# Performance work log

Measured on AMD Instinct MI355X. Metric: run time of the kernel, lower is better.

## Reference

```python
import jax, jax.numpy as jnp
import numpy as np

B, N_SIDE, S = 64, 40, 512
N = N_SIDE * N_SIDE          # 1600 grid points (fl_feature_dims [1,40,40])
EMB = 10                     # embedding_dim
GDIM = 8                     # lie('homography').dim
WIDTH = 128
C1 = 20                      # first-layer output channels


def _embed(x, emb_dim):
    # sinusoidal embedding of each scalar coordinate: [..., D] -> [..., D*emb_dim]
    freqs = 2.0 ** jnp.arange(emb_dim // 2, dtype=x.dtype)
    ang = x[..., None] * freqs                       # [..., D, emb/2]
    e = jnp.concatenate([jnp.sin(ang), jnp.cos(ang)], axis=-1)  # [..., D, emb]
    return e.reshape(x.shape[:-1] + (x.shape[-1] * emb_dim,))


def _glorot(key, shape):
    fan_in = shape[0]
    return jax.random.normal(key, shape, dtype=jnp.float32) / np.sqrt(fan_in)


def setup_inputs() -> dict:
    key = jax.random.key(0)
    ks = jax.random.split(key, 16)
    inp = {
        'data':   jax.random.normal(ks[0], (B, N, 1), dtype=jnp.float32),
        'v0':     jax.random.normal(ks[1], (S, GDIM), dtype=jnp.float32),
        'v_last': jax.random.normal(ks[2], (S, GDIM), dtype=jnp.float32),
        # FirstLayer filter MLP: 2*EMB -> 20 -> 20 -> 1*C1
        'fl_w1': _glorot(ks[3], (2 * EMB, 20)), 'fl_b1': jnp.zeros((20,), jnp.float32),
        'fl_w2': _glorot(ks[4], (20, 20)),      'fl_b2': jnp.zeros((20,), jnp.float32),
        'fl_w3': _glorot(ks[5], (20, C1)),      'fl_b3': jnp.zeros((C1,), jnp.float32),
        # Hidden FilterMLP: EMB*GDIM=80 -> WIDTH -> C1*WIDTH
        's_w1': _glorot(ks[6], (EMB * GDIM, WIDTH)), 's_b1': jnp.zeros((WIDTH,), jnp.float32),
        's_w2': _glorot(ks[7], (WIDTH, C1 * WIDTH)), 's_b2': jnp.zeros((C1 * WIDTH,), jnp.float32),
        'fc1_w': _glorot(ks[8], (WIDTH, WIDTH)), 'fc1_b': jnp.zeros((WIDTH,), jnp.float32),
        'fc2_w': _glorot(ks[9], (WIDTH, WIDTH)), 'fc2_b': jnp.zeros((WIDTH,), jnp.float32),
        'pool_w': _glorot(ks[10], (WIDTH, 10)),  'pool_b': jnp.zeros((10,), jnp.float32),
    }
    return inp


def reference(data, v0, v_last, fl_w1, fl_b1, fl_w2, fl_b2, fl_w3, fl_b3,
              s_w1, s_b1, s_w2, s_b2, fc1_w, fc1_b, fc2_w, fc2_b, pool_w, pool_b):
    silu = jax.nn.silu
    # pixel grid in [-1,1]^2, homogeneous coords [N,3]
    lin = jnp.linspace(-1.0, 1.0, N_SIDE, dtype=data.dtype)
    xx, yy = jnp.meshgrid(lin, lin, indexing='ij')
    coords = jnp.stack([xx.ravel(), yy.ravel()], axis=-1)           # [N,2]
    xh = jnp.concatenate([coords, jnp.ones((N, 1), data.dtype)], -1)  # [N,3]
    # homography matrices: identity + small perturbation from 8 group params
    pert = jnp.concatenate([0.1 * v_last, jnp.zeros((S, 1), data.dtype)], -1).reshape(S, 3, 3)
    H = jnp.eye(3, dtype=data.dtype) + pert                          # [S,3,3]
    y = jnp.einsum('sij,nj->sni', H, xh)                             # [S,N,3]
    t = y[..., :2] / y[..., 2:3]                                     # projective action [S,N,2]
    # continuous-kernel first layer: filters generated by MLP on embedded coords
    e1 = _embed(t, EMB)                                              # [S,N,20]
    h = silu(e1 @ fl_w1 + fl_b1)
    h = silu(h @ fl_w2 + fl_b2)
    filt1 = h @ fl_w3 + fl_b3                                        # [S,N,C1]
    z = jnp.einsum('bn,sno->bso', data[:, :, 0], filt1) / N          # [B,S,C1]
    z = silu(z)
    # hidden FilterMLP on group samples v0 -> per-sample filters [S,C1,WIDTH]
    v0e = _embed(v0, EMB)                                            # [S,80]
    h2 = silu(v0e @ s_w1 + s_b1)                                     # [S,WIDTH]
    filt2 = (h2 @ s_w2 + s_b2).reshape(S, C1, WIDTH)
    # (1/S) * sum over group-sample and channel axes of broadcast product
    z = jnp.einsum('bsc,scw->bw', z, filt2) / S                      # [B,WIDTH]
    z = silu(z @ fc1_w + fc1_b) + z
    z = silu(z @ fc2_w + fc2_b) + z
    return z @ pool_w + pool_b                                       # [B,10]
```

## Files before the change

### kernel.cpp

```cpp
#include <hip/hip_runtime.h>

#define N_PTS 1600
#define NSIDE 40
#define SNUM  512
#define BNUM  64
#define C1D   20
#define WID   128

typedef _Float16 h8  __attribute__((ext_vector_type(8)));
typedef _Float16 h4  __attribute__((ext_vector_type(4)));
typedef __fp16   h2v __attribute__((ext_vector_type(2)));
typedef float    f4  __attribute__((ext_vector_type(4)));

__device__ __forceinline__ float silu_f(float x){
    return x * __builtin_amdgcn_rcpf(1.f + __expf(-x));
}
__device__ __forceinline__ void fma4(float4& a, float s, const float4 w){
    a.x += s*w.x; a.y += s*w.y; a.z += s*w.z; a.w += s*w.w;
}

__global__ __launch_bounds__(256) void ka_prep(
    const float* __restrict__ data, const float* __restrict__ v0,
    const float* __restrict__ s_w1, const float* __restrict__ s_b1,
    const float* __restrict__ s_w2, const float* __restrict__ s_b2,
    const float* __restrict__ w1, const float* __restrict__ b1,
    const float* __restrict__ w2, const float* __restrict__ b2,
    const float* __restrict__ w3, const float* __restrict__ b3,
    _Float16* __restrict__ dataA, float* __restrict__ f2g,
    _Float16* __restrict__ wPackA, float* __restrict__ bPackA,
    float* __restrict__ out2g)
{
    const int t  = threadIdx.x;
    const int bx = blockIdx.x;
    if (bx == 690) {
        const float* wsrc[3] = { w1, w2, w3 };
        const float* bsrc[3] = { b1, b2, b3 };
        for (int v = t; v < 3072; v += 256) {
            const int l = v >> 10, rem = v & 1023;
            const int cout = rem >> 5, cin = rem & 31;
            float x = 0.f;
            if (cout < 20 && cin < 20) x = wsrc[l][cin * 20 + cout];
            wPackA[v] = (_Float16)x;
        }
        if (t < 96) {
            const int l = t >> 5, cout = t & 31;
            bPackA[t] = (cout < 20) ? bsrc[l][cout] : 0.f;
        }
        for (int v = t; v < 8192; v += 256) out2g[v] = 0.f;
        return;
    }
    if (bx >= 640) {
        const int o  = (bx - 640) * 256 + t;
        const int L  = o & 63, cm = o >> 6;
        const int mt = cm & 3, ch = cm >> 2;
        const int b  = mt * 16 + (L & 15);
        const int nb = ch * 32 + (L >> 4) * 8;
        const float* src = data + b * N_PTS + nb;
        h8 v;
        #pragma unroll
        for (int j = 0; j < 8; j++) v[j] = (_Float16)src[j];
        *(h8*)(dataA + (size_t)o * 8) = v;
        return;
    }
    const int st  = bx / 10, ct = bx - st * 10;
    const int s0  = st * 8;
    const int col = ct * 256 + t;
    __shared__ __align__(16) float h2t[128][12];
    __shared__ __align__(16) float svt[8][8][10];

    if (t < 64) {
        const int ss = t >> 3, d = t & 7;
        const float val = v0[(s0 + ss) * 8 + d];
        float sv, cv;
        __sincosf(val, &sv, &cv);
        #pragma unroll
        for (int k = 0; k < 5; k++) {
            svt[ss][d][k]     = sv;
            svt[ss][d][5 + k] = cv;
            const float ns = 2.f * sv * cv;
            const float nc = 1.f - 2.f * sv * sv;
            sv = ns; cv = nc;
        }
    }
    __syncthreads();

    {
        const int j  = t & 127;
        const int sh = t >> 7;
        float hacc[4];
        const float bias1 = s_b1[j];
        #pragma unroll
        for (int u = 0; u < 4; u++) hacc[u] = bias1;
        for (int d = 0; d < 8; d++) {
            #pragma unroll
            for (int kk = 0; kk < 10; kk++) {
                const float wv = s_w1[(d * 10 + kk) * WID + j];
                #pragma unroll
                for (int u = 0; u < 4; u++)
                    hacc[u] += svt[sh * 4 + u][d][kk] * wv;
            }
        }
        #pragma unroll
        for (int u = 0; u < 4; u++) h2t[j][sh * 4 + u] = silu_f(hacc[u]);
    }
    __syncthreads();

    float4 acc[2];
    acc[0] = make_float4(0.f, 0.f, 0.f, 0.f);
    acc[1] = make_float4(0.f, 0.f, 0.f, 0.f);
    #pragma unroll 4
    for (int i = 0; i < 128; i++) {
        const float wv = s_w2[i * 2560 + col];
        const float4* hh = (const float4*)&h2t[i][0];
        fma4(acc[0], wv, hh[0]);
        fma4(acc[1], wv, hh[1]);
    }
    const float bias = s_b2[col];
    const float* af = (const float*)acc;
    #pragma unroll
    for (int ss = 0; ss < 8; ss++)
        f2g[(s0 + ss) * 2560 + col] = af[ss] + bias;
}

__device__ __forceinline__ void embed_coord(
    int n, float hA, float hB, float hC, float h6, float h7, float h8c,
    h2v e5[5])
{
    const int i = n / NSIDE;
    const int j = n - i * NSIDE;
    const float x = -1.f + (float)i * (2.f/39.f);
    const float y = -1.f + (float)j * (2.f/39.f);
    const float yc = hA*x + hB*y + hC;
    const float y2 = h6*x + h7*y + h8c;
    const float tc = yc * __builtin_amdgcn_rcpf(y2);
    float e[10];
    float sv, cv;
    __sincosf(tc, &sv, &cv);
    #pragma unroll
    for (int k = 0; k < 5; k++) {
        e[k] = sv; e[5+k] = cv;
        const float ns = 2.f*sv*cv, nc = 1.f - 2.f*sv*sv; sv = ns; cv = nc;
    }
    #pragma unroll
    for (int k = 0; k < 5; k++)
        e5[k] = __builtin_amdgcn_cvt_pkrtz(e[2*k], e[2*k+1]);
}

#define ASTRIDE 40

__global__ __launch_bounds__(512, 8) void kf_filt(
    const float* __restrict__ v_last,
    const _Float16* __restrict__ wPackA, const float* __restrict__ bPackA,
    _Float16* __restrict__ filtG)
{
    const int s    = blockIdx.x & 511;
    const int half = blockIdx.x >> 9;
    const int nb0  = half * 800;
    const int t    = threadIdx.x;
    const int lane = t & 63;
    const int w    = t >> 6;
    const int q    = lane >> 4;
    const int l15  = lane & 15;
    const int ep   = lane >> 1;
    const int ec   = lane & 1;
    const int erow = w*16 + ep + ((ep >> 4) * 112);

    __shared__ __align__(16) _Float16 act[256 * ASTRIDE];
    __shared__ __align__(16) _Float16 wlds[3072];
    __shared__ __align__(16) float    blds[96];

    for (int v = t; v < 1536; v += 512)
        ((unsigned int*)wlds)[v] = ((const unsigned int*)wPackA)[v];
    if (t < 96) blds[t] = bPackA[t];

    float Hm[9];
    #pragma unroll
    for (int k = 0; k < 9; k++) Hm[k] = (k == 0 || k == 4 || k == 8) ? 1.f : 0.f;
    #pragma unroll
    for (int k = 0; k < 8; k++) Hm[k] += 0.1f * v_last[s*8 + k];
    const float hA = ec ? Hm[3] : Hm[0];
    const float hB = ec ? Hm[4] : Hm[1];
    const float hC = ec ? Hm[5] : Hm[2];

    if (ec == 0) {
        unsigned long long* pz = (unsigned long long*)(act + erow*ASTRIDE + 20);
        pz[0] = 0ull; pz[1] = 0ull; pz[2] = 0ull;
    }

    __syncthreads();

    _Float16* fgs = filtG + (size_t)(half*512 + s) * 16000;

    for (int base = 0; base < 800; base += 256) {
        const int tn = min(256, 800 - base);

        if (erow < tn) {
            h2v e5[5];
            embed_coord(nb0 + base + erow, hA, hB, hC, Hm[6], Hm[7], Hm[8], e5);
            #pragma unroll
            for (int k = 0; k < 5; k++)
                *(h2v*)(act + erow*ASTRIDE + ec*10 + 2*k) = e5[k];
        }

        const int nmt = tn >> 4;
        #pragma unroll
        for (int l = 0; l < 3; l++) {
            const h8 wf0 = *(const h8*)(wlds + ((l*2+0)*16 + l15) * 32 + q*8);
            const h8 wf1 = *(const h8*)(wlds + ((l*2+1)*16 + l15) * 32 + q*8);
            const float b0 = blds[(l*2+0)*16 + l15];
            const float b1 = blds[(l*2+1)*16 + l15];
            const f4 zero4 = (f4)(0.f);
            for (int mt = w; mt < nmt; mt += 8) {
                const int r0 = mt * 16;
                const h8 af = *(const h8*)(act + (r0 + l15)*ASTRIDE + q*8);
                f4 D0 = __builtin_amdgcn_mfma_f32_16x16x32_f16(af, wf0, zero4, 0, 0, 0);
                f4 D1 = __builtin_amdgcn_mfma_f32_16x16x32_f16(af, wf1, zero4, 0, 0, 0);
                if (l < 2) {
                    #pragma unroll
                    for (int r = 0; r < 4; r++) {
                        const int p = r0 + q*4 + r;
                        act[p*ASTRIDE + l15] = (_Float16)silu_f(D0[r] + b0);
                        if (l15 < 4)
                            act[p*ASTRIDE + 16 + l15] = (_Float16)silu_f(D1[r] + b1);
                    }
                } else {
                    h4 p0, p1;
                    #pragma unroll
                    for (int r = 0; r < 4; r++) {
                        p0[r] = (_Float16)(D0[r] + b0);
                        p1[r] = (_Float16)(D1[r] + b1);
                    }
                    *(h4*)(fgs + l15*800 + base + r0 + q*4) = p0;
                    if (l15 < 4)
                        *(h4*)(fgs + (16 + l15)*800 + base + r0 + q*4) = p1;
                }
            }
        }
    }
}

__global__ __launch_bounds__(256, 6) void kz_gemm(
    const _Float16* __restrict__ dataA, const _Float16* __restrict__ filtG,
    float* __restrict__ zpart)
{
    const int s    = blockIdx.x & 511;
    const int half = blockIdx.x >> 9;
    const int t    = threadIdx.x;
    const int lane = t & 63;
    const int w    = t >> 6;
    const int q    = lane >> 4;
    const int l15  = lane & 15;

    __shared__ __align__(16) float red[4 * 64 * 21];

    const _Float16* fgs = filtG + (size_t)(half*512 + s) * 16000;
    const int r1row = (l15 < 4) ? (16 + l15) : 0;

    f4 zacc[4][2];
    #pragma unroll
    for (int mt = 0; mt < 4; mt++) { zacc[mt][0] = (f4)(0.f); zacc[mt][1] = (f4)(0.f); }

    for (int kc = w; kc < 25; kc += 4) {
        const h8 bf0 = *(const h8*)(fgs + l15  *800 + kc*32 + q*8);
        const h8 bf1 = *(const h8*)(fgs + r1row*800 + kc*32 + q*8);
        const int gchunk = half*25 + kc;
        #pragma unroll
        for (int mt = 0; mt < 4; mt++) {
            const h8 afz = *(const h8*)(dataA + ((size_t)(gchunk*4 + mt)*64 + lane)*8);
            zacc[mt][0] = __builtin_amdgcn_mfma_f32_16x16x32_f16(afz, bf0, zacc[mt][0], 0, 0, 0);
            zacc[mt][1] = __builtin_amdgcn_mfma_f32_16x16x32_f16(afz, bf1, zacc[mt][1], 0, 0, 0);
        }
    }

    #pragma unroll
    for (int mt = 0; mt < 4; mt++) {
        #pragma unroll
        for (int r = 0; r < 4; r++) {
            const int b = mt*16 + q*4 + r;
            red[(w*64 + b)*21 + l15] = zacc[mt][0][r];
            if (l15 < 4) red[(w*64 + b)*21 + 16 + l15] = zacc[mt][1][r];
        }
    }
    __syncthreads();
    for (int v = t; v < 1280; v += 256) {
        const int c = v >> 6, b = v & 63;
        const float sum = red[(      b)*21 + c] + red[( 64 + b)*21 + c]
                        + red[(128 + b)*21 + c] + red[(192 + b)*21 + c];
        zpart[(half*512 + s)*1280 + v] = sum;
    }
}

__global__ __launch_bounds__(256) void k2_contract(
    const float* __restrict__ zg, const float* __restrict__ f2g,
    float* __restrict__ out2g)
{
    const int blk = blockIdx.x;
    const int sg  = blk >> 1;
    const int wh  = blk & 1;
    const int s0  = sg * 4;
    const int w0  = wh * 64;
    const int t   = threadIdx.x;
    __shared__ __align__(16) float zl[4*1280];
    __shared__ __align__(16) float fl[4*20*64];
    #pragma unroll
    for (int sp = 0; sp < 4; sp++) {
        const int srow = (s0 + sp) * 1280;
        for (int r = t; r < 1280; r += 256) {
            const float a0 = zg[srow + r];
            const float a1 = zg[512*1280 + srow + r];
            zl[sp*1280 + r] = silu_f((a0 + a1) * (1.f / (float)N_PTS));
        }
        for (int u = t; u < 1280; u += 256) {
            const int c = u >> 6, ww = u & 63;
            fl[sp*1280 + u] = f2g[(s0 + sp)*2560 + c*128 + w0 + ww];
        }
    }
    __syncthreads();
    const int ww = t & 63, bh = t >> 6;
    float4 acc[4];
    #pragma unroll
    for (int qq = 0; qq < 4; qq++) acc[qq] = make_float4(0.f, 0.f, 0.f, 0.f);
    #pragma unroll 4
    for (int sc = 0; sc < 80; sc++) {
        const float f = fl[sc * 64 + ww];
        const float4* zz = (const float4*)&zl[sc * 64 + bh * 16];
        #pragma unroll
        for (int qq = 0; qq < 4; qq++) fma4(acc[qq], f, zz[qq]);
    }
    const float* af = (const float*)acc;
    #pragma unroll
    for (int idx = 0; idx < 16; idx++) {
        const int b = bh * 16 + idx;
        atomicAdd(&out2g[b * 128 + w0 + ww], af[idx]);
    }
}

__global__ __launch_bounds__(128) void k3_tail(
    const float* __restrict__ out2g,
    const float* __restrict__ fc1w, const float* __restrict__ fc1b,
    const float* __restrict__ fc2w, const float* __restrict__ fc2b,
    const float* __restrict__ pw,   const float* __restrict__ pb,
    float* __restrict__ out)
{
    const int b = blockIdx.x, t = threadIdx.x;
    __shared__ float zb[128], r1[128], r2[128];
    zb[t] = out2g[b * 128 + t] * (1.f / (float)SNUM);
    __syncthreads();
    float a = fc1b[t];
    #pragma unroll 8
    for (int i = 0; i < 128; i++) a += zb[i] * fc1w[i * 128 + t];
    r1[t] = silu_f(a) + zb[t];
    __syncthreads();
    a = fc2b[t];
    #pragma unroll 8
    for (int i = 0; i < 128; i++) a += r1[i] * fc2w[i * 128 + t];
    r2[t] = silu_f(a) + r1[t];
    __syncthreads();
    if (t < 10) {
        float o = pb[t];
        #pragma unroll 8
        for (int i = 0; i < 128; i++) o += r2[i] * pw[i * 10 + t];
        out[b * 10 + t] = o;
    }
}

extern "C" void kernel_launch(void* const* d_in, const int* in_sizes, int n_in,
                              void* d_out, int out_size, void* d_ws, size_t ws_size,
                              hipStream_t stream) {
    const float* data   = (const float*)d_in[0];
    const float* v0     = (const float*)d_in[1];
    const float* v_last = (const float*)d_in[2];
    const float* fl_w1  = (const float*)d_in[3];
    const float* fl_b1  = (const float*)d_in[4];
    const float* fl_w2  = (const float*)d_in[5];
    const float* fl_b2  = (const float*)d_in[6];
    const float* fl_w3  = (const float*)d_in[7];
    const float* fl_b3  = (const float*)d_in[8];
    const float* s_w1   = (const float*)d_in[9];
    const float* s_b1   = (const float*)d_in[10];
    const float* s_w2   = (const float*)d_in[11];
    const float* s_b2   = (const float*)d_in[12];
    const float* fc1_w  = (const float*)d_in[13];
    const float* fc1_b  = (const float*)d_in[14];
    const float* fc2_w  = (const float*)d_in[15];
    const float* fc2_b  = (const float*)d_in[16];
    const float* pool_w = (const float*)d_in[17];
    const float* pool_b = (const float*)d_in[18];
    float* out = (float*)d_out;

    float* ws        = (float*)d_ws;
    _Float16* dataA  = (_Float16*)ws;
    float* zpart  = ws    + 51200;
    float* f2g    = zpart + 1310720;
    float* out2g  = f2g   + 1310720;
    _Float16* wPackA = (_Float16*)(out2g + 8192);
    float* bPackA = out2g + 8192 + 1536;
    _Float16* filtG = (_Float16*)(bPackA + 96);

    ka_prep    <<<691, 256, 0, stream>>>(data, v0, s_w1, s_b1, s_w2, s_b2,
                                         fl_w1, fl_b1, fl_w2, fl_b2, fl_w3, fl_b3,
                                         dataA, f2g, wPackA, bPackA, out2g);
    kf_filt    <<<1024, 512, 0, stream>>>(v_last, wPackA, bPackA, filtG);
    kz_gemm    <<<1024, 256, 0, stream>>>(dataA, filtG, zpart);
    k2_contract<<<256, 256, 0, stream>>>(zpart, f2g, out2g);
    k3_tail    <<<64, 128, 0, stream>>>(out2g, fc1_w, fc1_b, fc2_w, fc2_b,
                                        pool_w, pool_b, out);
}
```

Measured before the change: 180.2 us.

## Fuse prep kernel into filter kernel and split contraction across more blocks

Merges the prep work (hidden filter MLP, data fp16 packing, output zeroing) into the filter-generation kernel as extra blocks of one launch. Each filter block now packs the first-layer weights straight into LDS instead of reading a prepacked buffer, which removes one launch and the dependency between them. The contraction kernel is split over four width quarters instead of two, doubling its block count, and a GEMM loop gets an unroll hint. Each filter block now repeats the weight packing, and occupancy bounds drop from 8 to 6.

```diff
diff --git a/kernel.cpp b/kernel.cpp
--- a/kernel.cpp
+++ b/kernel.cpp
@@ -17,109 +17,6 @@
 }
 __device__ __forceinline__ void fma4(float4& a, float s, const float4 w){
     a.x += s*w.x; a.y += s*w.y; a.z += s*w.z; a.w += s*w.w;
-}
-
-__global__ __launch_bounds__(256) void ka_prep(
-    const float* __restrict__ data, const float* __restrict__ v0,
-    const float* __restrict__ s_w1, const float* __restrict__ s_b1,
-    const float* __restrict__ s_w2, const float* __restrict__ s_b2,
-    const float* __restrict__ w1, const float* __restrict__ b1,
-    const float* __restrict__ w2, const float* __restrict__ b2,
-    const float* __restrict__ w3, const float* __restrict__ b3,
-    _Float16* __restrict__ dataA, float* __restrict__ f2g,
-    _Float16* __restrict__ wPackA, float* __restrict__ bPackA,
-    float* __restrict__ out2g)
-{
-    const int t  = threadIdx.x;
-    const int bx = blockIdx.x;
-    if (bx == 690) {
-        const float* wsrc[3] = { w1, w2, w3 };
-        const float* bsrc[3] = { b1, b2, b3 };
-        for (int v = t; v < 3072; v += 256) {
-            const int l = v >> 10, rem = v & 1023;
-            const int cout = rem >> 5, cin = rem & 31;
-            float x = 0.f;
-            if (cout < 20 && cin < 20) x = wsrc[l][cin * 20 + cout];
-            wPackA[v] = (_Float16)x;
-        }
-        if (t < 96) {
-            const int l = t >> 5, cout = t & 31;
-            bPackA[t] = (cout < 20) ? bsrc[l][cout] : 0.f;
-        }
-        for (int v = t; v < 8192; v += 256) out2g[v] = 0.f;
-        return;
-    }
-    if (bx >= 640) {
-        const int o  = (bx - 640) * 256 + t;
-        const int L  = o & 63, cm = o >> 6;
-        const int mt = cm & 3, ch = cm >> 2;
-        const int b  = mt * 16 + (L & 15);
-        const int nb = ch * 32 + (L >> 4) * 8;
-        const float* src = data + b * N_PTS + nb;
-        h8 v;
-        #pragma unroll
-        for (int j = 0; j < 8; j++) v[j] = (_Float16)src[j];
-        *(h8*)(dataA + (size_t)o * 8) = v;
-        return;
-    }
-    const int st  = bx / 10, ct = bx - st * 10;
-    const int s0  = st * 8;
-    const int col = ct * 256 + t;
-    __shared__ __align__(16) float h2t[128][12];
-    __shared__ __align__(16) float svt[8][8][10];
-
-    if (t < 64) {
-        const int ss = t >> 3, d = t & 7;
-        const float val = v0[(s0 + ss) * 8 + d];
-        float sv, cv;
-        __sincosf(val, &sv, &cv);
-        #pragma unroll
-        for (int k = 0; k < 5; k++) {
-            svt[ss][d][k]     = sv;
-            svt[ss][d][5 + k] = cv;
-            const float ns = 2.f * sv * cv;
-            const float nc = 1.f - 2.f * sv * sv;
-            sv = ns; cv = nc;
-        }
-    }
-    __syncthreads();
-
-    {
-        const int j  = t & 127;
-        const int sh = t >> 7;
-        float hacc[4];
-        const float bias1 = s_b1[j];
-        #pragma unroll
-        for (int u = 0; u < 4; u++) hacc[u] = bias1;
-        for (int d = 0; d < 8; d++) {
-            #pragma unroll
-            for (int kk = 0; kk < 10; kk++) {
-                const float wv = s_w1[(d * 10 + kk) * WID + j];
-                #pragma unroll
-                for (int u = 0; u < 4; u++)
-                    hacc[u] += svt[sh * 4 + u][d][kk] * wv;
-            }
-        }
-        #pragma unroll
-        for (int u = 0; u < 4; u++) h2t[j][sh * 4 + u] = silu_f(hacc[u]);
-    }
-    __syncthreads();
-
-    float4 acc[2];
-    acc[0] = make_float4(0.f, 0.f, 0.f, 0.f);
-    acc[1] = make_float4(0.f, 0.f, 0.f, 0.f);
-    #pragma unroll 4
-    for (int i = 0; i < 128; i++) {
-        const float wv = s_w2[i * 2560 + col];
-        const float4* hh = (const float4*)&h2t[i][0];
-        fma4(acc[0], wv, hh[0]);
-        fma4(acc[1], wv, hh[1]);
-    }
-    const float bias = s_b2[col];
-    const float* af = (const float*)acc;
-    #pragma unroll
-    for (int ss = 0; ss < 8; ss++)
-        f2g[(s0 + ss) * 2560 + col] = af[ss] + bias;
 }
 
 __device__ __forceinline__ void embed_coord(
@@ -148,15 +45,100 @@
 
 #define ASTRIDE 40
 
-__global__ __launch_bounds__(512, 8) void kf_filt(
+__global__ __launch_bounds__(512, 6) void kaf_fused(
+    const float* __restrict__ data, const float* __restrict__ v0,
     const float* __restrict__ v_last,
-    const _Float16* __restrict__ wPackA, const float* __restrict__ bPackA,
-    _Float16* __restrict__ filtG)
+    const float* __restrict__ s_w1, const float* __restrict__ s_b1,
+    const float* __restrict__ s_w2, const float* __restrict__ s_b2,
+    const float* __restrict__ w1, const float* __restrict__ b1,
+    const float* __restrict__ w2, const float* __restrict__ b2,
+    const float* __restrict__ w3, const float* __restrict__ b3,
+    _Float16* __restrict__ dataA, float* __restrict__ f2g,
+    float* __restrict__ out2g, _Float16* __restrict__ filtG)
 {
-    const int s    = blockIdx.x & 511;
-    const int half = blockIdx.x >> 9;
+    const int t  = threadIdx.x;
+    const int bx = blockIdx.x;
+
+    __shared__ __align__(16) unsigned char smem[27008];
+
+    if (bx >= 1024) {
+        if (bx == 1689) {
+            for (int v = t; v < 8192; v += 512) out2g[v] = 0.f;
+            return;
+        }
+        if (bx >= 1664) {
+            const int o  = (bx - 1664) * 512 + t;
+            const int L  = o & 63, cm = o >> 6;
+            const int mt = cm & 3, ch = cm >> 2;
+            const int b  = mt * 16 + (L & 15);
+            const int nb = ch * 32 + (L >> 4) * 8;
+            const float* src = data + b * N_PTS + nb;
+            h8 v;
+            #pragma unroll
+            for (int j = 0; j < 8; j++) v[j] = (_Float16)src[j];
+            *(h8*)(dataA + (size_t)o * 8) = v;
+            return;
+        }
+        const int bxe = bx - 1024;
+        const int st  = bxe / 10, ct = bxe - st * 10;
+        const int s0  = st * 8;
+        float* h2t = (float*)smem;
+        float* svt = (float*)(smem + 6144);
+
+        if (t < 64) {
+            const int ss = t >> 3, d = t & 7;
+            const float val = v0[(s0 + ss) * 8 + d];
+            float sv, cv;
+            __sincosf(val, &sv, &cv);
+            #pragma unroll
+            for (int k = 0; k < 5; k++) {
+                svt[(ss*8 + d)*10 + k]     = sv;
+                svt[(ss*8 + d)*10 + 5 + k] = cv;
+                const float ns = 2.f * sv * cv;
+                const float nc = 1.f - 2.f * sv * sv;
+                sv = ns; cv = nc;
+            }
+        }
+        __syncthreads();
+
+        {
+            const int j  = t & 127;
+            const int sh = t >> 7;
+            const float bias1 = s_b1[j];
+            float h0 = bias1, h1 = bias1;
+            for (int d = 0; d < 8; d++) {
+                #pragma unroll
+                for (int kk = 0; kk < 10; kk++) {
+                    const float wv = s_w1[(d * 10 + kk) * WID + j];
+                    h0 += svt[((sh*2    )*8 + d)*10 + kk] * wv;
+                    h1 += svt[((sh*2 + 1)*8 + d)*10 + kk] * wv;
+                }
+            }
+            h2t[j*12 + sh*2    ] = silu_f(h0);
+            h2t[j*12 + sh*2 + 1] = silu_f(h1);
+        }
+        __syncthreads();
+
+        const int col = ct * 256 + (t & 255);
+        const int g   = t >> 8;
+        float4 acc = make_float4(0.f, 0.f, 0.f, 0.f);
+        #pragma unroll 4
+        for (int i = 0; i < 128; i++) {
+            const float wv = s_w2[i * 2560 + col];
+            const float4 hh = *(const float4*)&h2t[i*12 + g*4];
+            fma4(acc, wv, hh);
+        }
+        const float bias = s_b2[col];
+        const float* af = (const float*)&acc;
+        #pragma unroll
+        for (int u = 0; u < 4; u++)
+            f2g[(s0 + g*4 + u) * 2560 + col] = af[u] + bias;
+        return;
+    }
+
+    const int s    = bx & 511;
+    const int half = bx >> 9;
     const int nb0  = half * 800;
-    const int t    = threadIdx.x;
     const int lane = t & 63;
     const int w    = t >> 6;
     const int q    = lane >> 4;
@@ -165,13 +147,25 @@
     const int ec   = lane & 1;
     const int erow = w*16 + ep + ((ep >> 4) * 112);
 
-    __shared__ __align__(16) _Float16 act[256 * ASTRIDE];
-    __shared__ __align__(16) _Float16 wlds[3072];
-    __shared__ __align__(16) float    blds[96];
-
-    for (int v = t; v < 1536; v += 512)
-        ((unsigned int*)wlds)[v] = ((const unsigned int*)wPackA)[v];
-    if (t < 96) blds[t] = bPackA[t];
+    _Float16* act  = (_Float16*)smem;
+    _Float16* wlds = (_Float16*)(smem + 20480);
+    float*    blds = (float*)   (smem + 26624);
+
+    {
+        const float* wsrc[3] = { w1, w2, w3 };
+        const float* bsrc[3] = { b1, b2, b3 };
+        for (int v = t; v < 3072; v += 512) {
+            const int l = v >> 10, rem = v & 1023;
+            const int cout = rem >> 5, cin = rem & 31;
+            float x = 0.f;
+            if (cout < 20 && cin < 20) x = wsrc[l][cin * 20 + cout];
+            wlds[v] = (_Float16)x;
+        }
+        if (t < 96) {
+            const int l = t >> 5, cout = t & 31;
+            blds[t] = (cout < 20) ? bsrc[l][cout] : 0.f;
+        }
+    }
 
     float Hm[9];
     #pragma unroll
@@ -260,6 +254,7 @@
     #pragma unroll
     for (int mt = 0; mt < 4; mt++) { zacc[mt][0] = (f4)(0.f); zacc[mt][1] = (f4)(0.f); }
 
+    #pragma unroll 2
     for (int kc = w; kc < 25; kc += 4) {
         const h8 bf0 = *(const h8*)(fgs + l15  *800 + kc*32 + q*8);
         const h8 bf1 = *(const h8*)(fgs + r1row*800 + kc*32 + q*8);
@@ -295,13 +290,13 @@
     float* __restrict__ out2g)
 {
     const int blk = blockIdx.x;
-    const int sg  = blk >> 1;
-    const int wh  = blk & 1;
+    const int sg  = blk >> 2;
+    const int wq  = blk & 3;
     const int s0  = sg * 4;
-    const int w0  = wh * 64;
+    const int w0  = wq * 32;
     const int t   = threadIdx.x;
     __shared__ __align__(16) float zl[4*1280];
-    __shared__ __align__(16) float fl[4*20*64];
+    __shared__ __align__(16) float fl[4*20*32];
     #pragma unroll
     for (int sp = 0; sp < 4; sp++) {
         const int srow = (s0 + sp) * 1280;
@@ -310,27 +305,27 @@
             const float a1 = zg[512*1280 + srow + r];
             zl[sp*1280 + r] = silu_f((a0 + a1) * (1.f / (float)N_PTS));
         }
-        for (int u = t; u < 1280; u += 256) {
-            const int c = u >> 6, ww = u & 63;
-            fl[sp*1280 + u] = f2g[(s0 + sp)*2560 + c*128 + w0 + ww];
-        }
-    }
-    __syncthreads();
-    const int ww = t & 63, bh = t >> 6;
-    float4 acc[4];
-    #pragma unroll
-    for (int qq = 0; qq < 4; qq++) acc[qq] = make_float4(0.f, 0.f, 0.f, 0.f);
+        for (int u = t; u < 640; u += 256) {
+            const int c = u >> 5, ww = u & 31;
+            fl[sp*640 + u] = f2g[(s0 + sp)*2560 + c*128 + w0 + ww];
+        }
+    }
+    __syncthreads();
+    const int ww = t & 31, bh = t >> 5;
+    float4 acc[2];
+    acc[0] = make_float4(0.f, 0.f, 0.f, 0.f);
+    acc[1] = make_float4(0.f, 0.f, 0.f, 0.f);
     #pragma unroll 4
     for (int sc = 0; sc < 80; sc++) {
-        const float f = fl[sc * 64 + ww];
-        const float4* zz = (const float4*)&zl[sc * 64 + bh * 16];
-        #pragma unroll
-        for (int qq = 0; qq < 4; qq++) fma4(acc[qq], f, zz[qq]);
+        const float f = fl[sc * 32 + ww];
+        const float4* zz = (const float4*)&zl[sc * 64 + bh * 8];
+        fma4(acc[0], f, zz[0]);
+        fma4(acc[1], f, zz[1]);
     }
     const float* af = (const float*)acc;
     #pragma unroll
-    for (int idx = 0; idx < 16; idx++) {
-        const int b = bh * 16 + idx;
+    for (int idx = 0; idx < 8; idx++) {
+        const int b = bh * 8 + idx;
         atomicAdd(&out2g[b * 128 + w0 + ww], af[idx]);
     }
 }
@@ -393,16 +388,14 @@
     float* zpart  = ws    + 51200;
     float* f2g    = zpart + 1310720;
     float* out2g  = f2g   + 1310720;
-    _Float16* wPackA = (_Float16*)(out2g + 8192);
-    float* bPackA = out2g + 8192 + 1536;
-    _Float16* filtG = (_Float16*)(bPackA + 96);
-
-    ka_prep    <<<691, 256, 0, stream>>>(data, v0, s_w1, s_b1, s_w2, s_b2,
-                                         fl_w1, fl_b1, fl_w2, fl_b2, fl_w3, fl_b3,
-                                         dataA, f2g, wPackA, bPackA, out2g);
-    kf_filt    <<<1024, 512, 0, stream>>>(v_last, wPackA, bPackA, filtG);
+    _Float16* filtG = (_Float16*)(out2g + 8192);
+
+    kaf_fused  <<<1690, 512, 0, stream>>>(data, v0, v_last,
+                                          s_w1, s_b1, s_w2, s_b2,
+                                          fl_w1, fl_b1, fl_w2, fl_b2, fl_w3, fl_b3,
+                                          dataA, f2g, out2g, filtG);
     kz_gemm    <<<1024, 256, 0, stream>>>(dataA, filtG, zpart);
-    k2_contract<<<256, 256, 0, stream>>>(zpart, f2g, out2g);
+    k2_contract<<<512, 256, 0, stream>>>(zpart, f2g, out2g);
     k3_tail    <<<64, 128, 0, stream>>>(out2g, fc1_w, fc1_b, fc2_w, fc2_b,
                                         pool_w, pool_b, out);
 }
```

Result: faster. 168.3 us (-6.6%).
